# Kernel optimization log

Hardware: AMD Instinct MI355X
Metric: run time of the kernel (lower is better)

## Reference

```python
import jax, jax.numpy as jnp
import numpy as np

N_NODES = 50000
N_EDGES = 800000
D = 128
H = 8
HD = D // H
N_NTYPES = 3
N_ETYPES = 5
LN_EPS = 1e-5


def setup_inputs() -> dict:
    key = jax.random.key(0)
    ks = jax.random.split(key, 16)
    inp = {
        "x": jax.random.normal(ks[0], (N_NODES, D), dtype=jnp.float32),
        "edge_index": jax.random.randint(ks[1], (2, N_EDGES), 0, N_NODES),
        "edge_type": jax.random.randint(ks[2], (N_EDGES,), 0, N_ETYPES),
        "node_type": jax.random.randint(ks[3], (N_NODES,), 0, N_NTYPES),
        # per-(node_type, head) QKV projections, per-(edge_type, head) K transform
        "W_Q": jax.random.normal(ks[4], (N_NTYPES, H, HD, HD), dtype=jnp.float32) * 0.02,
        "W_K": jax.random.normal(ks[5], (N_NTYPES, H, HD, HD), dtype=jnp.float32) * 0.02,
        "W_V": jax.random.normal(ks[6], (N_NTYPES, H, HD, HD), dtype=jnp.float32) * 0.02,
        "W_edge": jax.random.normal(ks[7], (N_ETYPES, H, HD, HD), dtype=jnp.float32) * 0.02,
        "mu": jnp.ones((H, N_ETYPES), dtype=jnp.float32),
        "W_out": jax.random.normal(ks[8], (D, D), dtype=jnp.float32) * 0.02,
        "b_out": jnp.zeros((D,), dtype=jnp.float32),
        "ln1_g": jnp.ones((D,), dtype=jnp.float32),
        "ln1_b": jnp.zeros((D,), dtype=jnp.float32),
        "W1": jax.random.normal(ks[9], (D, 4 * D), dtype=jnp.float32) * 0.02,
        "b1": jnp.zeros((4 * D,), dtype=jnp.float32),
        "W2": jax.random.normal(ks[10], (4 * D, D), dtype=jnp.float32) * 0.02,
        "b2": jnp.zeros((D,), dtype=jnp.float32),
        "ln2_g": jnp.ones((D,), dtype=jnp.float32),
        "ln2_b": jnp.zeros((D,), dtype=jnp.float32),
    }
    return inp


def _layer_norm(y, g, b):
    m = y.mean(-1, keepdims=True)
    v = ((y - m) ** 2).mean(-1, keepdims=True)
    return (y - m) * jax.lax.rsqrt(v + LN_EPS) * g + b


def reference(x, edge_index, edge_type, node_type,
              W_Q, W_K, W_V, W_edge, mu,
              W_out, b_out, ln1_g, ln1_b, W1, b1, W2, b2, ln2_g, ln2_b):
    N = x.shape[0]
    xh = x.reshape(N, H, HD)  # heads vectorized (concat of per-head slices)

    # type-specific QKV: small fixed loop over node types, masked select
    Q = jnp.zeros_like(xh)
    K = jnp.zeros_like(xh)
    V = jnp.zeros_like(xh)
    for t in range(N_NTYPES):
        m = (node_type == t)[:, None, None]
        Q = jnp.where(m, jnp.einsum('nhd,hdf->nhf', xh, W_Q[t]), Q)
        K = jnp.where(m, jnp.einsum('nhd,hdf->nhf', xh, W_K[t]), K)
        V = jnp.where(m, jnp.einsum('nhd,hdf->nhf', xh, W_V[t]), V)

    src, dst = edge_index[0], edge_index[1]
    q_dst = Q[dst]   # [E,H,HD]
    k_src = K[src]   # [E,H,HD]

    # edge-type-specific K transform
    kt = jnp.zeros_like(k_src)
    for et in range(N_ETYPES):
        m = (edge_type == et)[:, None, None]
        kt = jnp.where(m, jnp.einsum('ehd,hdf->ehf', k_src, W_edge[et]), kt)

    scores = (q_dst * kt).sum(-1) / jnp.sqrt(jnp.float32(HD))  # [E,H]
    scores = scores * mu[:, edge_type].T                       # mu per edge type, per head

    # sparse softmax over incoming edges of each dst node, per head
    smax = jax.ops.segment_max(scores, dst, num_segments=N)
    ex = jnp.exp(scores - smax[dst])
    den = jax.ops.segment_sum(ex, dst, num_segments=N)
    w = ex / (den[dst] + 1e-10)                                 # [E,H]

    agg = jax.ops.segment_sum(V[src] * w[..., None], dst, num_segments=N)  # [N,H,HD]
    mh = agg.reshape(N, D) @ W_out + b_out  # dropout is identity in eval

    h = _layer_norm(x + mh, ln1_g, ln1_b)
    ffn = jax.nn.gelu(h @ W1 + b1, approximate=False) @ W2 + b2
    return _layer_norm(h + ffn, ln2_g, ln2_b)
```

## Files before the change

### kernel.cpp

```cpp
#include <hip/hip_runtime.h>
#include <hip/hip_bf16.h>

#define N_NODESC 50000
#define N_EDGESC 800000
#define DD 128
#define HH 8
#define HDIM 16
#define N_NT 3
#define N_ET 5
#define NPB 196
#define NEB 400
#define NFB 512

#define KV8_OFF    ((size_t)0)
#define QT8_OFF    ((size_t)12800000)
#define XP_OFF     ((size_t)44800000)
#define AGG_OFF    ((size_t)57600000)
#define WOUTT_OFF  ((size_t)83200000)
#define W1T_OFF    ((size_t)83232768)
#define W2T_OFF    ((size_t)83363840)
#define WALL_OFF   ((size_t)83494912)
#define EDATA_OFF  ((size_t)84183040)
#define ROWS_OFF   ((size_t)87383040)
#define ORIG_OFF   ((size_t)87583104)
#define DEG_OFF    ((size_t)87783104)
#define TOFS_OFF   ((size_t)87983104)
#define BH_OFF     ((size_t)87983168)
#define BB_OFF     ((size_t)87985536)
#define TMP_OFF    ((size_t)87988928)
#define RLOC_OFF   ((size_t)91188928)
#define CSUM_OFF   ((size_t)91389056)

using short8 = __attribute__((ext_vector_type(8))) short;
using f32x4  = __attribute__((ext_vector_type(4))) float;
using f32x2  = __attribute__((ext_vector_type(2))) float;

__device__ __forceinline__ ushort f2b(float f) {
    __hip_bfloat16 h = __float2bfloat16(f);
    return *(ushort*)&h;
}
__device__ __forceinline__ float b2f(ushort u) {
    __hip_bfloat16 h = *(__hip_bfloat16*)&u;
    return __bfloat162float(h);
}
__device__ __forceinline__ f32x2 pk0(unsigned int w) {
    return __builtin_amdgcn_cvt_pk_f32_fp8((int)w, false);
}
__device__ __forceinline__ f32x2 pk1(unsigned int w) {
    return __builtin_amdgcn_cvt_pk_f32_fp8((int)w, true);
}
__device__ __forceinline__ float gelu_f(float v) {
    return 0.5f * v * (1.f + erff(v * 0.70710678118654752f));
}
__device__ __forceinline__ void ebar() {
    __builtin_amdgcn_sched_barrier(0);
    asm volatile("s_waitcnt lgkmcnt(0)" ::: "memory");
    __builtin_amdgcn_sched_barrier(0);
    __builtin_amdgcn_s_barrier();
    __builtin_amdgcn_sched_barrier(0);
}

__global__ __launch_bounds__(256) void prep_a(
    const float* __restrict__ Wout, const float* __restrict__ W1, const float* __restrict__ W2,
    const float* __restrict__ WQ, const float* __restrict__ Wk, const float* __restrict__ Wv,
    const float* __restrict__ We, const float* __restrict__ mu,
    ushort* __restrict__ Woutt, ushort* __restrict__ W1t, ushort* __restrict__ W2t,
    ushort* __restrict__ Wall,
    const int* __restrict__ ntype, int* __restrict__ bh,
    const int* __restrict__ dst, int* __restrict__ deg, unsigned int* __restrict__ tmp)
{
    const int b = blockIdx.x, tid = threadIdx.x;
    if (b < 1920) {
        const int gid = b * 256 + tid;
        if (gid < 16384) {
            const int nn = gid >> 7, k = gid & 127;
            Woutt[gid] = f2b(Wout[k * 128 + nn]);
        } else if (gid < 81920) {
            const int i = gid - 16384;
            const int nn = i >> 7, k = i & 127;
            W1t[i] = f2b(W1[k * 512 + nn]);
        } else if (gid < 147456) {
            const int i = gid - 81920;
            const int nn = i >> 9, k = i & 511;
            W2t[i] = f2b(W2[k * 128 + nn]);
        } else {
            const int idx = gid - 147456;
            const int t = idx / (896 * 128);
            const int rem = idx % (896 * 128);
            const int c = rem / 128, k = rem % 128;
            const int hk = k >> 4, ck = k & 15;
            float v = 0.f;
            if (c < 128) {
                const int hc = c >> 4, j = c & 15;
                if (hk == hc) v = 4.f * Wk[((t * HH + hc) * HDIM + ck) * HDIM + j];
            } else if (c < 256) {
                const int c2 = c - 128, hc = c2 >> 4, j = c2 & 15;
                if (hk == hc) v = 4.f * Wv[((t * HH + hc) * HDIM + ck) * HDIM + j];
            } else {
                const int cq = c - 256, et = cq >> 7, dd = cq & 127;
                const int hq = dd >> 4, j = dd & 15;
                if (hk == hq) {
                    const float* wq = WQ + ((t * HH + hq) * HDIM + ck) * HDIM;
                    const float* we = We + ((et * HH + hq) * HDIM + j) * HDIM;
                    float s = 0.f;
#pragma unroll
                    for (int f = 0; f < 16; f++) s = fmaf(wq[f], we[f], s);
                    v = 64.f * mu[hq * N_ET + et] * s;
                }
            }
            Wall[idx] = f2b(v);
        }
    } else if (b < 1920 + NPB) {
        const int bc = b - 1920;
        const int wave = tid >> 6, lane = tid & 63;
        const int n = bc * 256 + tid;
        const int t = (n < N_NODESC) ? ntype[n] : -1;
        const unsigned long long m0 = __ballot(t == 0);
        const unsigned long long m1 = __ballot(t == 1);
        const unsigned long long m2 = __ballot(t == 2);
        __shared__ int wcnt[4][3];
        if (lane == 0) {
            wcnt[wave][0] = (int)__popcll(m0);
            wcnt[wave][1] = (int)__popcll(m1);
            wcnt[wave][2] = (int)__popcll(m2);
        }
        __syncthreads();
        if (tid < 3)
            bh[tid * NPB + bc] = wcnt[0][tid] + wcnt[1][tid] + wcnt[2][tid] + wcnt[3][tid];
    } else {
        for (int e = (b - 1920 - NPB) * 256 + tid; e < N_EDGESC; e += NEB * 256) {
            const int nd = dst[e];
            const unsigned int p = (unsigned int)atomicAdd(&deg[nd], 1);
            tmp[e] = (p << 16) | (unsigned int)nd;
        }
    }
}

__global__ __launch_bounds__(256) void prep_b(
    const int* __restrict__ bh, const int* __restrict__ deg,
    int* __restrict__ bb, int* __restrict__ tofs,
    int* __restrict__ rloc, int* __restrict__ csum)
{
    __shared__ int part[256];
    const int tid = threadIdx.x;
    if (blockIdx.x == 0) {
        const int base3 = tid * 3;
        int e0 = (base3 + 0 < 588) ? bh[base3 + 0] : 0;
        int e1 = (base3 + 1 < 588) ? bh[base3 + 1] : 0;
        int e2 = (base3 + 2 < 588) ? bh[base3 + 2] : 0;
        const int l0 = e0, l1 = e0 + e1, l2 = l1 + e2;
        part[tid] = l2;
        __syncthreads();
        for (int off = 1; off < 256; off <<= 1) {
            const int u = (tid >= off) ? part[tid - off] : 0;
            __syncthreads();
            part[tid] += u;
            __syncthreads();
        }
        const int tb = part[tid] - l2;
        if (base3 + 0 < 588) bb[base3 + 0] = tb;
        if (base3 + 1 < 588) bb[base3 + 1] = tb + l0;
        if (base3 + 2 < 588) bb[base3 + 2] = tb + l1;
        __syncthreads();
        if (tid == 0) {
            tofs[0] = 0;
            tofs[1] = bb[NPB];
            tofs[2] = bb[2 * NPB];
            tofs[3] = N_NODESC;
        }
    } else {
        const int c = blockIdx.x - 1;
        const int n = c * 256 + tid;
        const int vdeg = (n < N_NODESC) ? deg[n] : 0;
        part[tid] = vdeg;
        __syncthreads();
        for (int off = 1; off < 256; off <<= 1) {
            const int u = (tid >= off) ? part[tid - off] : 0;
            __syncthreads();
            part[tid] += u;
            __syncthreads();
        }
        if (n <= N_NODESC) rloc[n] = part[tid] - vdeg;
        if (tid == 255) csum[c] = part[255];
    }
}

__global__ __launch_bounds__(256) void prep_c(
    const int* __restrict__ ntype, const float* __restrict__ x,
    const int* __restrict__ src, const int* __restrict__ etype,
    const int* __restrict__ bb, const int* __restrict__ rloc, const int* __restrict__ csum,
    const unsigned int* __restrict__ tmp,
    int* __restrict__ origof, ushort* __restrict__ Xp, int* __restrict__ rows,
    int* __restrict__ edata)
{
    const int b = blockIdx.x, tid = threadIdx.x;
    __shared__ int cb[256];
    {
        const int v = (tid < NPB) ? csum[tid] : 0;
        cb[tid] = v;
        __syncthreads();
        for (int off = 1; off < 256; off <<= 1) {
            const int u = (tid >= off) ? cb[tid - off] : 0;
            __syncthreads();
            cb[tid] += u;
            __syncthreads();
        }
        const int incl = cb[tid];
        __syncthreads();
        cb[tid] = incl - v;
        __syncthreads();
    }

    if (b < NPB) {
        const int wave = tid >> 6, lane = tid & 63;
        const int n = b * 256 + tid;
        const int t = (n < N_NODESC) ? ntype[n] : -1;
        const unsigned long long m0 = __ballot(t == 0);
        const unsigned long long m1 = __ballot(t == 1);
        const unsigned long long m2 = __ballot(t == 2);
        __shared__ int wcnt[4][3];
        __shared__ int sp[256];
        if (lane == 0) {
            wcnt[wave][0] = (int)__popcll(m0);
            wcnt[wave][1] = (int)__popcll(m1);
            wcnt[wave][2] = (int)__popcll(m2);
        }
        __syncthreads();
        int p = -1;
        if (n < N_NODESC) {
            int basew = 0;
#pragma unroll
            for (int w = 0; w < 4; w++) if (w < wave) basew += wcnt[w][t];
            const unsigned long long mt = (t == 0) ? m0 : (t == 1) ? m1 : m2;
            const unsigned long long mlt = ((unsigned long long)1 << lane) - 1;
            p = bb[t * NPB + b] + basew + (int)__popcll(mt & mlt);
            origof[p] = n;
        }
        if (n <= N_NODESC) rows[n] = cb[b] + rloc[n];
        sp[tid] = p;
        __syncthreads();
        for (int i = tid; i < 256 * 16; i += 256) {
            const int nn = i >> 4, c = (i & 15) << 3;
            const int pp = sp[nn];
            if (pp < 0) continue;
            const int n2 = b * 256 + nn;
            const float4 v0 = *(const float4*)(x + (size_t)n2 * DD + c);
            const float4 v1 = *(const float4*)(x + (size_t)n2 * DD + c + 4);
            ushort o[8] = {f2b(v0.x), f2b(v0.y), f2b(v0.z), f2b(v0.w),
                           f2b(v1.x), f2b(v1.y), f2b(v1.z), f2b(v1.w)};
            *(uint4*)(Xp + (size_t)pp * DD + c) = *(uint4*)o;
        }
    } else {
        for (int e = (b - NPB) * 256 + tid; e < N_EDGESC; e += NFB * 256) {
            const unsigned int v = tmp[e];
            const int nd = (int)(v & 0xffffu);
            const int p = (int)(v >> 16);
            edata[cb[nd >> 8] + rloc[nd] + p] = src[e] | (etype[e] << 16);
        }
    }
}

#define LDP 36

__global__ __launch_bounds__(256) void proj_gemm(
    const ushort* __restrict__ Xp, const ushort* __restrict__ Wall,
    const int* __restrict__ tofs, const int* __restrict__ origof,
    ushort* __restrict__ KV8, unsigned char* __restrict__ Qt8)
{
    const int t = blockIdx.z;
    const int rs = tofs[t], re = tofs[t + 1];
    const int mBase = rs + blockIdx.x * 128;
    if (mBase >= re) return;
    const int nBase = blockIdx.y * 128;
    const ushort* Bt = Wall + (size_t)t * 896 * 128;

    __shared__ ushort As[128 * LDP];
    __shared__ ushort Bs[128 * LDP];
    const int tid = threadIdx.x;
    const int lane = tid & 63, wave = tid >> 6;
    const int mw = (wave >> 1) * 64, nw = (wave & 1) * 64;
    const int l15 = lane & 15, q8 = (lane >> 4) * 8;

    f32x4 acc[4][4];
#pragma unroll
    for (int i = 0; i < 4; i++)
#pragma unroll
        for (int j = 0; j < 4; j++) acc[i][j] = (f32x4){0.f, 0.f, 0.f, 0.f};

    const int r0 = tid >> 2, c0 = (tid & 3) * 8;
    int rA0 = mBase + r0;      if (rA0 >= N_NODESC) rA0 = N_NODESC - 1;
    int rA1 = mBase + r0 + 64; if (rA1 >= N_NODESC) rA1 = N_NODESC - 1;

    for (int kk = 0; kk < 128; kk += 32) {
        short8 a0 = *(const short8*)(Xp + (size_t)rA0 * DD + kk + c0);
        short8 a1 = *(const short8*)(Xp + (size_t)rA1 * DD + kk + c0);
        short8 b0 = *(const short8*)(Bt + (size_t)(nBase + r0) * 128 + kk + c0);
        short8 b1 = *(const short8*)(Bt + (size_t)(nBase + r0 + 64) * 128 + kk + c0);
        *(short8*)&As[r0 * LDP + c0] = a0;
        *(short8*)&As[(r0 + 64) * LDP + c0] = a1;
        *(short8*)&Bs[r0 * LDP + c0] = b0;
        *(short8*)&Bs[(r0 + 64) * LDP + c0] = b1;
        __syncthreads();
        short8 af[4], bf[4];
#pragma unroll
        for (int i = 0; i < 4; i++)
            af[i] = *(const short8*)&As[(mw + i * 16 + l15) * LDP + q8];
#pragma unroll
        for (int j = 0; j < 4; j++)
            bf[j] = *(const short8*)&Bs[(nw + j * 16 + l15) * LDP + q8];
#pragma unroll
        for (int i = 0; i < 4; i++)
#pragma unroll
            for (int j = 0; j < 4; j++)
                acc[i][j] = __builtin_amdgcn_mfma_f32_16x16x32_bf16(af[i], bf[j], acc[i][j], 0, 0, 0);
        __syncthreads();
    }

    unsigned char* kvb = (unsigned char*)KV8;
    const int rq = (lane >> 4) * 4;
#pragma unroll
    for (int i = 0; i < 4; i++) {
#pragma unroll
        for (int r = 0; r < 4; r++) {
            const int gm = mBase + mw + i * 16 + rq + r;
            if (gm >= re) continue;
            const int og = origof[gm];
#pragma unroll
            for (int j = 0; j < 4; j++) {
                const int gn = nBase + nw + j * 16 + l15;
                const float v = acc[i][j][r];
                const unsigned char b8 =
                    (unsigned char)(__builtin_amdgcn_cvt_pk_fp8_f32(v, v, 0, false) & 0xff);
                if (gn < 256) kvb[(size_t)og * 256 + gn] = b8;
                else          Qt8[(size_t)og * 640 + (gn - 256)] = b8;
            }
        }
    }
}

__global__ __launch_bounds__(128) void edgeagg_kernel(
    const int* __restrict__ rowstart, const int* __restrict__ edata,
    const unsigned char* __restrict__ Qt8, const unsigned char* __restrict__ KV8,
    ushort* __restrict__ agg)
{
    const int w = threadIdx.x >> 6;
    const int lane = threadIdx.x & 63;
    const int n = blockIdx.x * 2 + w;
    const int slot = lane >> 3;
    const int h = lane & 7;

    __shared__ uint4 qs8s[2][40];
    if (lane < 40)
        qs8s[w][lane] = ((const uint4*)(Qt8 + (size_t)n * 640))[lane];
    __syncthreads();
    const uint* qbase = (const uint*)&qs8s[w][0];

    const int s0 = rowstart[n], s1 = rowstart[n + 1];
    const float qsc = 1.44269504f / 1024.f;

    float acc[16];
#pragma unroll
    for (int j = 0; j < 16; j++) acc[j] = 0.f;
    float den = 0.f;

    for (int i = s0 + slot; i < s1; i += 8) {
        const int ed = edata[i];
        const int sn = ed & 0xffff;
        const int et = ed >> 16;
        const unsigned char* kvp = KV8 + ((size_t)sn << 8);
        const uint4 kw = *(const uint4*)(kvp + (h << 4));
        const uint4 vw = *(const uint4*)(kvp + 128 + (h << 4));
        const uint4 qw = *(const uint4*)(qbase + (et << 5) + (h << 2));

        const f32x2 q0 = pk0(qw.x), q1 = pk1(qw.x), q2 = pk0(qw.y), q3 = pk1(qw.y);
        const f32x2 q4 = pk0(qw.z), q5 = pk1(qw.z), q6 = pk0(qw.w), q7 = pk1(qw.w);
        const f32x2 k0 = pk0(kw.x), k1 = pk1(kw.x), k2 = pk0(kw.y), k3 = pk1(kw.y);
        const f32x2 k4 = pk0(kw.z), k5 = pk1(kw.z), k6 = pk0(kw.w), k7 = pk1(kw.w);

        float pa = q0.x * k0.x;
        float pb = q0.y * k0.y;
        float pc = q1.x * k1.x;
        float pd = q1.y * k1.y;
        pa = fmaf(q2.x, k2.x, pa); pb = fmaf(q2.y, k2.y, pb);
        pc = fmaf(q3.x, k3.x, pc); pd = fmaf(q3.y, k3.y, pd);
        pa = fmaf(q4.x, k4.x, pa); pb = fmaf(q4.y, k4.y, pb);
        pc = fmaf(q5.x, k5.x, pc); pd = fmaf(q5.y, k5.y, pd);
        pa = fmaf(q6.x, k6.x, pa); pb = fmaf(q6.y, k6.y, pb);
        pc = fmaf(q7.x, k7.x, pc); pd = fmaf(q7.y, k7.y, pd);

        const float ex = exp2f(((pa + pb) + (pc + pd)) * qsc);
        den += ex;

        const f32x2 v0 = pk0(vw.x), v1 = pk1(vw.x), v2 = pk0(vw.y), v3 = pk1(vw.y);
        const f32x2 v4 = pk0(vw.z), v5 = pk1(vw.z), v6 = pk0(vw.w), v7 = pk1(vw.w);
        acc[0]  = fmaf(ex, v0.x, acc[0]);  acc[1]  = fmaf(ex, v0.y, acc[1]);
        acc[2]  = fmaf(ex, v1.x, acc[2]);  acc[3]  = fmaf(ex, v1.y, acc[3]);
        acc[4]  = fmaf(ex, v2.x, acc[4]);  acc[5]  = fmaf(ex, v2.y, acc[5]);
        acc[6]  = fmaf(ex, v3.x, acc[6]);  acc[7]  = fmaf(ex, v3.y, acc[7]);
        acc[8]  = fmaf(ex, v4.x, acc[8]);  acc[9]  = fmaf(ex, v4.y, acc[9]);
        acc[10] = fmaf(ex, v5.x, acc[10]); acc[11] = fmaf(ex, v5.y, acc[11]);
        acc[12] = fmaf(ex, v6.x, acc[12]); acc[13] = fmaf(ex, v6.y, acc[13]);
        acc[14] = fmaf(ex, v7.x, acc[14]); acc[15] = fmaf(ex, v7.y, acc[15]);
    }

    {
        const int b0 = slot & 1, b1 = slot & 2, b2 = slot & 4;
#pragma unroll
        for (int j = 0; j < 8; j++) {
            const float v = b0 ? acc[j] : acc[j + 8];
            const float r = __shfl_xor(v, 8);
            acc[j] = (b0 ? acc[j + 8] : acc[j]) + r;
        }
#pragma unroll
        for (int j = 0; j < 4; j++) {
            const float v = b1 ? acc[j] : acc[j + 4];
            const float r = __shfl_xor(v, 16);
            acc[j] = (b1 ? acc[j + 4] : acc[j]) + r;
        }
#pragma unroll
        for (int j = 0; j < 2; j++) {
            const float v = b2 ? acc[j] : acc[j + 2];
            const float r = __shfl_xor(v, 32);
            acc[j] = (b2 ? acc[j + 2] : acc[j]) + r;
        }
        den += __shfl_xor(den, 8);
        den += __shfl_xor(den, 16);
        den += __shfl_xor(den, 32);
    }
    const float rr = 0.25f / (den + 1e-10f);
    const int fb = (h << 4) + ((slot & 1) << 3) + ((slot & 2) << 1) + ((slot & 4) >> 1);
    ushort o2[2] = { f2b(acc[0] * rr), f2b(acc[1] * rr) };
    *(uint*)&agg[((size_t)n << 7) + fb] = *(uint*)o2;
}

#define LDH 132

__global__ __launch_bounds__(256) void fused_tail(
    const ushort* __restrict__ agg, const ushort* __restrict__ Woutt,
    const ushort* __restrict__ W1t, const ushort* __restrict__ W2t,
    const float* __restrict__ x,
    const float* __restrict__ bout, const float* __restrict__ g1, const float* __restrict__ b1ln,
    const float* __restrict__ b1, const float* __restrict__ b2,
    const float* __restrict__ g2, const float* __restrict__ b2ln,
    float* __restrict__ out)
{
    __shared__ ushort As[64 * LDP];
    __shared__ ushort Bs[128 * LDP];
    __shared__ ushort Hs[64 * LDH];
    __shared__ ushort Ts[64 * LDH];
    __shared__ float red[2][2][64];

    const int tid = threadIdx.x;
    const int lane = tid & 63, wave = tid >> 6;
    const int wm = wave >> 1, wn = wave & 1;
    const int l15 = lane & 15, q8 = (lane >> 4) * 8, rq = (lane >> 4) * 4;
    const int mBase = blockIdx.x * 64;

    const int r0 = tid >> 2, c0 = (tid & 3) * 8;
    int rowA = mBase + r0; if (rowA >= N_NODESC) rowA = N_NODESC - 1;

    f32x4 acc1[2][4], acc2[2][4];
#pragma unroll
    for (int i = 0; i < 2; i++)
#pragma unroll
        for (int j = 0; j < 4; j++) {
            acc1[i][j] = (f32x4){0.f, 0.f, 0.f, 0.f};
            acc2[i][j] = (f32x4){0.f, 0.f, 0.f, 0.f};
        }

    short8 pA, pB0, pB1;
    pA  = *(const short8*)(agg + (size_t)rowA * DD + c0);
    pB0 = *(const short8*)(Woutt + (size_t)r0 * 128 + c0);
    pB1 = *(const short8*)(Woutt + (size_t)(r0 + 64) * 128 + c0);

    for (int kk = 0; kk < 4; kk++) {
        ebar();
        *(short8*)&As[r0 * LDP + c0] = pA;
        *(short8*)&Bs[r0 * LDP + c0] = pB0;
        *(short8*)&Bs[(r0 + 64) * LDP + c0] = pB1;
        if (kk < 3) {
            pA  = *(const short8*)(agg + (size_t)rowA * DD + (kk + 1) * 32 + c0);
            pB0 = *(const short8*)(Woutt + (size_t)r0 * 128 + (kk + 1) * 32 + c0);
            pB1 = *(const short8*)(Woutt + (size_t)(r0 + 64) * 128 + (kk + 1) * 32 + c0);
        } else {
            pB0 = *(const short8*)(W1t + (size_t)r0 * 128 + c0);
            pB1 = *(const short8*)(W1t + (size_t)(r0 + 64) * 128 + c0);
        }
        ebar();
        short8 af[2], bf[4];
#pragma unroll
        for (int i = 0; i < 2; i++)
            af[i] = *(const short8*)&As[(wm * 32 + i * 16 + l15) * LDP + q8];
#pragma unroll
        for (int j = 0; j < 4; j++)
            bf[j] = *(const short8*)&Bs[(wn * 64 + j * 16 + l15) * LDP + q8];
#pragma unroll
        for (int i = 0; i < 2; i++)
#pragma unroll
            for (int j = 0; j < 4; j++)
                acc1[i][j] = __builtin_amdgcn_mfma_f32_16x16x32_bf16(af[i], bf[j], acc1[i][j], 0, 0, 0);
    }

    {
        float boutv[4], gv[4], bv[4];
#pragma unroll
        for (int j = 0; j < 4; j++) {
            const int gn = wn * 64 + j * 16 + l15;
            boutv[j] = bout[gn]; gv[j] = g1[gn]; bv[j] = b1ln[gn];
        }
#pragma unroll
        for (int i = 0; i < 2; i++) {
#pragma unroll
            for (int r = 0; r < 4; r++) {
                const int row = wm * 32 + i * 16 + rq + r;
                const int gm = mBase + row;
                const int gr = (gm < N_NODESC) ? gm : N_NODESC - 1;
                float s = 0.f, ss = 0.f;
#pragma unroll
                for (int j = 0; j < 4; j++) {
                    const int gn = wn * 64 + j * 16 + l15;
                    float v = acc1[i][j][r] + boutv[j] + x[(size_t)gr * DD + gn];
                    acc1[i][j][r] = v;
                    s += v; ss += v * v;
                }
                s  += __shfl_xor(s, 1);  s  += __shfl_xor(s, 2);  s  += __shfl_xor(s, 4);  s  += __shfl_xor(s, 8);
                ss += __shfl_xor(ss, 1); ss += __shfl_xor(ss, 2); ss += __shfl_xor(ss, 4); ss += __shfl_xor(ss, 8);
                if (l15 == 0) { red[0][wn][row] = s; red[1][wn][row] = ss; }
            }
        }
        ebar();
#pragma unroll
        for (int i = 0; i < 2; i++) {
#pragma unroll
            for (int r = 0; r < 4; r++) {
                const int row = wm * 32 + i * 16 + rq + r;
                const float s  = red[0][0][row] + red[0][1][row];
                const float ss = red[1][0][row] + red[1][1][row];
                const float mean = s * (1.f / 128.f);
                const float var  = ss * (1.f / 128.f) - mean * mean;
                const float rstd = rsqrtf(var + 1e-5f);
#pragma unroll
                for (int j = 0; j < 4; j++) {
                    const int gn = wn * 64 + j * 16 + l15;
                    Hs[row * LDH + gn] = f2b((acc1[i][j][r] - mean) * rstd * gv[j] + bv[j]);
                }
            }
        }
    }

    for (int nb = 0; nb < 4; nb++) {
        f32x4 a1[2][4];
#pragma unroll
        for (int i = 0; i < 2; i++)
#pragma unroll
            for (int j = 0; j < 4; j++) a1[i][j] = (f32x4){0.f, 0.f, 0.f, 0.f};

        for (int kk = 0; kk < 4; kk++) {
            ebar();
            *(short8*)&Bs[r0 * LDP + c0] = pB0;
            *(short8*)&Bs[(r0 + 64) * LDP + c0] = pB1;
            if (kk < 3) {
                pB0 = *(const short8*)(W1t + (size_t)(nb * 128 + r0) * 128 + (kk + 1) * 32 + c0);
                pB1 = *(const short8*)(W1t + (size_t)(nb * 128 + r0 + 64) * 128 + (kk + 1) * 32 + c0);
            } else {
                pB0 = *(const short8*)(W2t + (size_t)r0 * 512 + nb * 128 + c0);
                pB1 = *(const short8*)(W2t + (size_t)(r0 + 64) * 512 + nb * 128 + c0);
            }
            ebar();
            short8 af[2], bf[4];
#pragma unroll
            for (int i = 0; i < 2; i++)
                af[i] = *(const short8*)&Hs[(wm * 32 + i * 16 + l15) * LDH + kk * 32 + q8];
#pragma unroll
            for (int j = 0; j < 4; j++)
                bf[j] = *(const short8*)&Bs[(wn * 64 + j * 16 + l15) * LDP + q8];
#pragma unroll
            for (int i = 0; i < 2; i++)
#pragma unroll
                for (int j = 0; j < 4; j++)
                    a1[i][j] = __builtin_amdgcn_mfma_f32_16x16x32_bf16(af[i], bf[j], a1[i][j], 0, 0, 0);
        }

        {
            float b1v[4];
#pragma unroll
            for (int j = 0; j < 4; j++)
                b1v[j] = b1[nb * 128 + wn * 64 + j * 16 + l15];
#pragma unroll
            for (int i = 0; i < 2; i++)
#pragma unroll
                for (int j = 0; j < 4; j++)
#pragma unroll
                    for (int r = 0; r < 4; r++) {
                        const int row = wm * 32 + i * 16 + rq + r;
                        const int col = wn * 64 + j * 16 + l15;
                        Ts[row * LDH + col] = f2b(gelu_f(a1[i][j][r] + b1v[j]));
                    }
        }

        for (int kk = 0; kk < 4; kk++) {
            ebar();
            *(short8*)&Bs[r0 * LDP + c0] = pB0;
            *(short8*)&Bs[(r0 + 64) * LDP + c0] = pB1;
            if (kk < 3) {
                pB0 = *(const short8*)(W2t + (size_t)r0 * 512 + nb * 128 + (kk + 1) * 32 + c0);
                pB1 = *(const short8*)(W2t + (size_t)(r0 + 64) * 512 + nb * 128 + (kk + 1) * 32 + c0);
            } else if (nb < 3) {
                pB0 = *(const short8*)(W1t + (size_t)((nb + 1) * 128 + r0) * 128 + c0);
                pB1 = *(const short8*)(W1t + (size_t)((nb + 1) * 128 + r0 + 64) * 128 + c0);
            }
            ebar();
            short8 af[2], bf[4];
#pragma unroll
            for (int i = 0; i < 2; i++)
                af[i] = *(const short8*)&Ts[(wm * 32 + i * 16 + l15) * LDH + kk * 32 + q8];
#pragma unroll
            for (int j = 0; j < 4; j++)
                bf[j] = *(const short8*)&Bs[(wn * 64 + j * 16 + l15) * LDP + q8];
#pragma unroll
            for (int i = 0; i < 2; i++)
#pragma unroll
                for (int j = 0; j < 4; j++)
                    acc2[i][j] = __builtin_amdgcn_mfma_f32_16x16x32_bf16(af[i], bf[j], acc2[i][j], 0, 0, 0);
        }
    }

    {
        float b2v[4], gv[4], bv[4];
#pragma unroll
        for (int j = 0; j < 4; j++) {
            const int gn = wn * 64 + j * 16 + l15;
            b2v[j] = b2[gn]; gv[j] = g2[gn]; bv[j] = b2ln[gn];
        }
        ebar();
#pragma unroll
        for (int i = 0; i < 2; i++) {
#pragma unroll
            for (int r = 0; r < 4; r++) {
                const int row = wm * 32 + i * 16 + rq + r;
                float s = 0.f, ss = 0.f;
#pragma unroll
                for (int j = 0; j < 4; j++) {
                    const int gn = wn * 64 + j * 16 + l15;
                    float v = acc2[i][j][r] + b2v[j] + b2f(Hs[row * LDH + gn]);
                    acc2[i][j][r] = v;
                    s += v; ss += v * v;
                }
                s  += __shfl_xor(s, 1);  s  += __shfl_xor(s, 2);  s  += __shfl_xor(s, 4);  s  += __shfl_xor(s, 8);
                ss += __shfl_xor(ss, 1); ss += __shfl_xor(ss, 2); ss += __shfl_xor(ss, 4); ss += __shfl_xor(ss, 8);
                if (l15 == 0) { red[0][wn][row] = s; red[1][wn][row] = ss; }
            }
        }
        ebar();
#pragma unroll
        for (int i = 0; i < 2; i++) {
#pragma unroll
            for (int r = 0; r < 4; r++) {
                const int row = wm * 32 + i * 16 + rq + r;
                const int gm = mBase + row;
                if (gm >= N_NODESC) continue;
                const float s  = red[0][0][row] + red[0][1][row];
                const float ss = red[1][0][row] + red[1][1][row];
                const float mean = s * (1.f / 128.f);
                const float var  = ss * (1.f / 128.f) - mean * mean;
                const float rstd = rsqrtf(var + 1e-5f);
#pragma unroll
                for (int j = 0; j < 4; j++) {
                    const int gn = wn * 64 + j * 16 + l15;
                    out[(size_t)gm * DD + gn] = (acc2[i][j][r] - mean) * rstd * gv[j] + bv[j];
                }
            }
        }
    }
}

extern "C" void kernel_launch(void* const* d_in, const int* in_sizes, int n_in,
                              void* d_out, int out_size, void* d_ws, size_t ws_size,
                              hipStream_t stream)
{
    const float* x     = (const float*)d_in[0];
    const int*   ei    = (const int*)d_in[1];
    const int*   etyp  = (const int*)d_in[2];
    const int*   ntype = (const int*)d_in[3];
    const float* Wq    = (const float*)d_in[4];
    const float* Wk    = (const float*)d_in[5];
    const float* Wv    = (const float*)d_in[6];
    const float* We    = (const float*)d_in[7];
    const float* mu    = (const float*)d_in[8];
    const float* Wout  = (const float*)d_in[9];
    const float* bout  = (const float*)d_in[10];
    const float* g1    = (const float*)d_in[11];
    const float* b1ln  = (const float*)d_in[12];
    const float* W1    = (const float*)d_in[13];
    const float* b1    = (const float*)d_in[14];
    const float* W2    = (const float*)d_in[15];
    const float* b2    = (const float*)d_in[16];
    const float* g2    = (const float*)d_in[17];
    const float* b2ln  = (const float*)d_in[18];
    float* out = (float*)d_out;

    char* ws = (char*)d_ws;
    ushort*        KV8   = (ushort*)(ws + KV8_OFF);
    unsigned char* Qt8   = (unsigned char*)(ws + QT8_OFF);
    ushort*        Xp    = (ushort*)(ws + XP_OFF);
    ushort*        agg   = (ushort*)(ws + AGG_OFF);
    ushort*        Woutt = (ushort*)(ws + WOUTT_OFF);
    ushort*        W1t   = (ushort*)(ws + W1T_OFF);
    ushort*        W2t   = (ushort*)(ws + W2T_OFF);
    ushort*        Wall  = (ushort*)(ws + WALL_OFF);
    int*           edata = (int*)(ws + EDATA_OFF);
    int*           rows  = (int*)(ws + ROWS_OFF);
    int*           origof= (int*)(ws + ORIG_OFF);
    int*           deg   = (int*)(ws + DEG_OFF);
    int*           tofs  = (int*)(ws + TOFS_OFF);
    int*           bh    = (int*)(ws + BH_OFF);
    int*           bb    = (int*)(ws + BB_OFF);
    unsigned int*  tmp   = (unsigned int*)(ws + TMP_OFF);
    int*           rloc  = (int*)(ws + RLOC_OFF);
    int*           csum  = (int*)(ws + CSUM_OFF);

    const int* srcA = ei;
    const int* dstA = ei + N_EDGESC;

    (void)hipMemsetAsync(ws + DEG_OFF, 0, 200000, stream);

    prep_a<<<1920 + NPB + NEB, 256, 0, stream>>>(
        Wout, W1, W2, Wq, Wk, Wv, We, mu, Woutt, W1t, W2t, Wall,
        ntype, bh, dstA, deg, tmp);
    prep_b<<<1 + NPB, 256, 0, stream>>>(bh, deg, bb, tofs, rloc, csum);
    prep_c<<<NPB + NFB, 256, 0, stream>>>(ntype, x, srcA, etyp, bb, rloc, csum, tmp,
                                          origof, Xp, rows, edata);

    proj_gemm<<<dim3(394, 7, 3), 256, 0, stream>>>(Xp, Wall, tofs, origof, KV8, Qt8);
    edgeagg_kernel<<<N_NODESC / 2, 128, 0, stream>>>(rows, edata, Qt8,
                                                     (const unsigned char*)KV8, agg);

    fused_tail<<<782, 256, 0, stream>>>(agg, Woutt, W1t, W2t, x,
                                        bout, g1, b1ln, b1, b2, g2, b2ln, out);
}
```

Baseline: 324.8 us.

## Stage full 128-wide K tiles in fused tail to cut barriers

The fused tail kernel now stages each whole 128x128 weight tile (and the 64x128 agg tile, reusing Ts) into shared memory at once, instead of four 32-wide K slices with two barriers each. Each GEMM now takes one barrier pair rather than eight. The next weight tile is prefetched into registers while the current one is consumed. It also preloads the residual x values into registers at kernel start. This cuts synchronisation and exposed global-load latency, but raises register use (12 short8 prefetch buffers plus 32 floats of x) and the shared-memory footprint, which may reduce occupancy.

```diff
diff --git a/kernel.cpp b/kernel.cpp
--- a/kernel.cpp
+++ b/kernel.cpp
@@ -434,6 +434,7 @@
 }
 
 #define LDH 132
+#define LDB 132
 
 __global__ __launch_bounds__(256) void fused_tail(
     const ushort* __restrict__ agg, const ushort* __restrict__ Woutt,
@@ -444,8 +445,7 @@
     const float* __restrict__ g2, const float* __restrict__ b2ln,
     float* __restrict__ out)
 {
-    __shared__ ushort As[64 * LDP];
-    __shared__ ushort Bs[128 * LDP];
+    __shared__ ushort Bs[128 * LDB];
     __shared__ ushort Hs[64 * LDH];
     __shared__ ushort Ts[64 * LDH];
     __shared__ float red[2][2][64];
@@ -459,6 +459,25 @@
     const int r0 = tid >> 2, c0 = (tid & 3) * 8;
     int rowA = mBase + r0; if (rowA >= N_NODESC) rowA = N_NODESC - 1;
 
+    short8 pA[4], pB0[4], pB1[4];
+#pragma unroll
+    for (int kk = 0; kk < 4; kk++) {
+        pA[kk]  = *(const short8*)(agg + (size_t)rowA * DD + kk * 32 + c0);
+        pB0[kk] = *(const short8*)(Woutt + (size_t)r0 * 128 + kk * 32 + c0);
+        pB1[kk] = *(const short8*)(Woutt + (size_t)(r0 + 64) * 128 + kk * 32 + c0);
+    }
+    float xv[2][4][4];
+#pragma unroll
+    for (int i = 0; i < 2; i++)
+#pragma unroll
+        for (int r = 0; r < 4; r++) {
+            const int gm = mBase + wm * 32 + i * 16 + rq + r;
+            const int gr = (gm < N_NODESC) ? gm : N_NODESC - 1;
+#pragma unroll
+            for (int j = 0; j < 4; j++)
+                xv[i][r][j] = x[(size_t)gr * DD + wn * 64 + j * 16 + l15];
+        }
+
     f32x4 acc1[2][4], acc2[2][4];
 #pragma unroll
     for (int i = 0; i < 2; i++)
@@ -468,32 +487,27 @@
             acc2[i][j] = (f32x4){0.f, 0.f, 0.f, 0.f};
         }
 
-    short8 pA, pB0, pB1;
-    pA  = *(const short8*)(agg + (size_t)rowA * DD + c0);
-    pB0 = *(const short8*)(Woutt + (size_t)r0 * 128 + c0);
-    pB1 = *(const short8*)(Woutt + (size_t)(r0 + 64) * 128 + c0);
-
+#pragma unroll
     for (int kk = 0; kk < 4; kk++) {
-        ebar();
-        *(short8*)&As[r0 * LDP + c0] = pA;
-        *(short8*)&Bs[r0 * LDP + c0] = pB0;
-        *(short8*)&Bs[(r0 + 64) * LDP + c0] = pB1;
-        if (kk < 3) {
-            pA  = *(const short8*)(agg + (size_t)rowA * DD + (kk + 1) * 32 + c0);
-            pB0 = *(const short8*)(Woutt + (size_t)r0 * 128 + (kk + 1) * 32 + c0);
-            pB1 = *(const short8*)(Woutt + (size_t)(r0 + 64) * 128 + (kk + 1) * 32 + c0);
-        } else {
-            pB0 = *(const short8*)(W1t + (size_t)r0 * 128 + c0);
-            pB1 = *(const short8*)(W1t + (size_t)(r0 + 64) * 128 + c0);
-        }
-        ebar();
+        *(short8*)&Ts[r0 * LDH + kk * 32 + c0] = pA[kk];
+        *(short8*)&Bs[r0 * LDB + kk * 32 + c0] = pB0[kk];
+        *(short8*)&Bs[(r0 + 64) * LDB + kk * 32 + c0] = pB1[kk];
+    }
+#pragma unroll
+    for (int kk = 0; kk < 4; kk++) {
+        pB0[kk] = *(const short8*)(W1t + (size_t)r0 * 128 + kk * 32 + c0);
+        pB1[kk] = *(const short8*)(W1t + (size_t)(r0 + 64) * 128 + kk * 32 + c0);
+    }
+    ebar();
+#pragma unroll
+    for (int kk = 0; kk < 4; kk++) {
         short8 af[2], bf[4];
 #pragma unroll
         for (int i = 0; i < 2; i++)
-            af[i] = *(const short8*)&As[(wm * 32 + i * 16 + l15) * LDP + q8];
+            af[i] = *(const short8*)&Ts[(wm * 32 + i * 16 + l15) * LDH + kk * 32 + q8];
 #pragma unroll
         for (int j = 0; j < 4; j++)
-            bf[j] = *(const short8*)&Bs[(wn * 64 + j * 16 + l15) * LDP + q8];
+            bf[j] = *(const short8*)&Bs[(wn * 64 + j * 16 + l15) * LDB + kk * 32 + q8];
 #pragma unroll
         for (int i = 0; i < 2; i++)
 #pragma unroll
@@ -513,13 +527,10 @@
 #pragma unroll
             for (int r = 0; r < 4; r++) {
                 const int row = wm * 32 + i * 16 + rq + r;
-                const int gm = mBase + row;
-                const int gr = (gm < N_NODESC) ? gm : N_NODESC - 1;
                 float s = 0.f, ss = 0.f;
 #pragma unroll
                 for (int j = 0; j < 4; j++) {
-                    const int gn = wn * 64 + j * 16 + l15;
-                    float v = acc1[i][j][r] + boutv[j] + x[(size_t)gr * DD + gn];
+                    float v = acc1[i][j][r] + boutv[j] + xv[i][r][j];
                     acc1[i][j][r] = v;
                     s += v; ss += v * v;
                 }
@@ -549,31 +560,32 @@
     }
 
     for (int nb = 0; nb < 4; nb++) {
+        ebar();
+#pragma unroll
+        for (int kk = 0; kk < 4; kk++) {
+            *(short8*)&Bs[r0 * LDB + kk * 32 + c0] = pB0[kk];
+            *(short8*)&Bs[(r0 + 64) * LDB + kk * 32 + c0] = pB1[kk];
+        }
+#pragma unroll
+        for (int kk = 0; kk < 4; kk++) {
+            pB0[kk] = *(const short8*)(W2t + (size_t)r0 * 512 + nb * 128 + kk * 32 + c0);
+            pB1[kk] = *(const short8*)(W2t + (size_t)(r0 + 64) * 512 + nb * 128 + kk * 32 + c0);
+        }
+        ebar();
         f32x4 a1[2][4];
 #pragma unroll
         for (int i = 0; i < 2; i++)
 #pragma unroll
             for (int j = 0; j < 4; j++) a1[i][j] = (f32x4){0.f, 0.f, 0.f, 0.f};
-
+#pragma unroll
         for (int kk = 0; kk < 4; kk++) {
-            ebar();
-            *(short8*)&Bs[r0 * LDP + c0] = pB0;
-            *(short8*)&Bs[(r0 + 64) * LDP + c0] = pB1;
-            if (kk < 3) {
-                pB0 = *(const short8*)(W1t + (size_t)(nb * 128 + r0) * 128 + (kk + 1) * 32 + c0);
-                pB1 = *(const short8*)(W1t + (size_t)(nb * 128 + r0 + 64) * 128 + (kk + 1) * 32 + c0);
-            } else {
-                pB0 = *(const short8*)(W2t + (size_t)r0 * 512 + nb * 128 + c0);
-                pB1 = *(const short8*)(W2t + (size_t)(r0 + 64) * 512 + nb * 128 + c0);
-            }
-            ebar();
             short8 af[2], bf[4];
 #pragma unroll
             for (int i = 0; i < 2; i++)
                 af[i] = *(const short8*)&Hs[(wm * 32 + i * 16 + l15) * LDH + kk * 32 + q8];
 #pragma unroll
             for (int j = 0; j < 4; j++)
-                bf[j] = *(const short8*)&Bs[(wn * 64 + j * 16 + l15) * LDP + q8];
+                bf[j] = *(const short8*)&Bs[(wn * 64 + j * 16 + l15) * LDB + kk * 32 + q8];
 #pragma unroll
             for (int i = 0; i < 2; i++)
 #pragma unroll
@@ -581,6 +593,7 @@
                     a1[i][j] = __builtin_amdgcn_mfma_f32_16x16x32_bf16(af[i], bf[j], a1[i][j], 0, 0, 0);
         }
 
+        ebar();
         {
             float b1v[4];
 #pragma unroll
@@ -597,26 +610,28 @@
                         Ts[row * LDH + col] = f2b(gelu_f(a1[i][j][r] + b1v[j]));
                     }
         }
-
+#pragma unroll
         for (int kk = 0; kk < 4; kk++) {
-            ebar();
-            *(short8*)&Bs[r0 * LDP + c0] = pB0;
-            *(short8*)&Bs[(r0 + 64) * LDP + c0] = pB1;
-            if (kk < 3) {
-                pB0 = *(const short8*)(W2t + (size_t)r0 * 512 + nb * 128 + (kk + 1) * 32 + c0);
-                pB1 = *(const short8*)(W2t + (size_t)(r0 + 64) * 512 + nb * 128 + (kk + 1) * 32 + c0);
-            } else if (nb < 3) {
-                pB0 = *(const short8*)(W1t + (size_t)((nb + 1) * 128 + r0) * 128 + c0);
-                pB1 = *(const short8*)(W1t + (size_t)((nb + 1) * 128 + r0 + 64) * 128 + c0);
+            *(short8*)&Bs[r0 * LDB + kk * 32 + c0] = pB0[kk];
+            *(short8*)&Bs[(r0 + 64) * LDB + kk * 32 + c0] = pB1[kk];
+        }
+        if (nb < 3) {
+#pragma unroll
+            for (int kk = 0; kk < 4; kk++) {
+                pB0[kk] = *(const short8*)(W1t + (size_t)((nb + 1) * 128 + r0) * 128 + kk * 32 + c0);
+                pB1[kk] = *(const short8*)(W1t + (size_t)((nb + 1) * 128 + r0 + 64) * 128 + kk * 32 + c0);
             }
-            ebar();
+        }
+        ebar();
+#pragma unroll
+        for (int kk = 0; kk < 4; kk++) {
             short8 af[2], bf[4];
 #pragma unroll
             for (int i = 0; i < 2; i++)
                 af[i] = *(const short8*)&Ts[(wm * 32 + i * 16 + l15) * LDH + kk * 32 + q8];
 #pragma unroll
             for (int j = 0; j < 4; j++)
-                bf[j] = *(const short8*)&Bs[(wn * 64 + j * 16 + l15) * LDP + q8];
+                bf[j] = *(const short8*)&Bs[(wn * 64 + j * 16 + l15) * LDB + kk * 32 + q8];
 #pragma unroll
             for (int i = 0; i < 2; i++)
 #pragma unroll
@@ -632,7 +647,6 @@
             const int gn = wn * 64 + j * 16 + l15;
             b2v[j] = b2[gn]; gv[j] = g2[gn]; bv[j] = b2ln[gn];
         }
-        ebar();
 #pragma unroll
         for (int i = 0; i < 2; i++) {
 #pragma unroll
```

After: 317.7 us. 2.2% less time.
